# Optimization experiments

Hardware: AMD Instinct MI355X
Metric: run time of the kernel (lower is better)

## Reference

```python
import jax, jax.numpy as jnp
import numpy as np

B, S, H, NH = 2, 2048, 2048, 16
HD = H // NH  # 128
SCALE = HD ** -0.5


def rotate_half(x):
    x1, x2 = x[..., : x.shape[-1] // 2], x[..., x.shape[-1] // 2 :]
    return jnp.concatenate((-x2, x1), axis=-1)


def setup_inputs() -> dict:
    key = jax.random.key(0)
    ks = jax.random.split(key, 7)
    inv_freq = 1.0 / (10000.0 ** (np.arange(0, HD, 2, dtype=np.float32) / HD))
    t = np.arange(S, dtype=np.float32)
    freqs = np.outer(t, inv_freq)  # [S, HD/2]
    emb = np.concatenate([freqs, freqs], axis=-1)  # [S, HD]
    cos = jnp.asarray(np.cos(emb))[None, None]  # [1,1,S,HD]
    sin = jnp.asarray(np.sin(emb))[None, None]
    std = H ** -0.5
    return {
        "hidden_states": jax.random.normal(ks[0], (B, S, H), jnp.float32),
        "cos": cos,
        "sin": sin,
        "Wq": jax.random.normal(ks[1], (H, H), jnp.float32) * std,
        "Wk": jax.random.normal(ks[2], (H, H), jnp.float32) * std,
        "Wv": jax.random.normal(ks[3], (H, H), jnp.float32) * std,
        "Wo": jax.random.normal(ks[4], (H, H), jnp.float32) * std,
    }


def reference(hidden_states, cos, sin, Wq, Wk, Wv, Wo):
    b, s, _ = hidden_states.shape
    # projections (torch F.linear: x @ W.T), reshape to [b, nh, s, hd]
    def proj(W):
        y = jnp.einsum("bsh,oh->bso", hidden_states, W)
        return y.reshape(b, s, NH, HD).transpose(0, 2, 1, 3)

    q, k, v = proj(Wq), proj(Wk), proj(Wv)
    # rotary embedding
    q = q * cos + rotate_half(q) * sin
    k = k * cos + rotate_half(k) * sin
    # attention: scores [b, nh, s, s]
    scores = jnp.einsum("bhqd,bhkd->bhqk", q, k) * SCALE
    causal_mask = jnp.triu(jnp.full((s, s), -jnp.inf, dtype=scores.dtype), k=1)
    scores = scores + causal_mask
    attn = jax.nn.softmax(scores, axis=-1)
    out = jnp.einsum("bhqk,bhkd->bhqd", attn, v)
    out = out.transpose(0, 2, 1, 3).reshape(b, s, NH * HD)
    return jnp.einsum("bso,ho->bsh", out, Wo)
```

## Files before the change

### kernel.cpp

```cpp
#include <hip/hip_runtime.h>

typedef unsigned short u16;
typedef unsigned int   u32;
typedef __attribute__((ext_vector_type(8))) __bf16 bf16x8;
typedef __attribute__((ext_vector_type(8))) unsigned short u16x8;
typedef __attribute__((ext_vector_type(4))) float f32x4;

#define DEVINL static __device__ __forceinline__
#define MFMA16(a,b,c) __builtin_amdgcn_mfma_f32_16x16x32_bf16((a),(b),(c),0,0,0)

#define GLOAD16(g, l) __builtin_amdgcn_global_load_lds( \
    (const __attribute__((address_space(1))) void*)(g), \
    (__attribute__((address_space(3))) void*)(l), 16, 0, 0)

constexpr float ATT_SCALE = 0.08838834764831845f;

DEVINL u16 f2bf(float f) {
  union { float f; u32 u; } v; v.f = f;
  u32 r = v.u + 0x7fffu + ((v.u >> 16) & 1u);
  return (u16)(r >> 16);
}

struct CvtArgs {
  const float* src[5];
  u16*         dst[5];
  int          nblk[5];
};

__global__ __launch_bounds__(256) void cvt_bf16(CvtArgs a) {
  const int z = blockIdx.y;
  if (blockIdx.x >= a.nblk[z]) return;
  const size_t i = ((size_t)blockIdx.x * 256 + threadIdx.x) * 8;
  const float* s = a.src[z] + i;
  float4 x0 = *(const float4*)(s);
  float4 x1 = *(const float4*)(s + 4);
  u16x8 r;
  r[0]=f2bf(x0.x); r[1]=f2bf(x0.y); r[2]=f2bf(x0.z); r[3]=f2bf(x0.w);
  r[4]=f2bf(x1.x); r[5]=f2bf(x1.y); r[6]=f2bf(x1.z); r[7]=f2bf(x1.w);
  *(u16x8*)(a.dst[z] + i) = r;
}

#define SLOT_U16 24576
#define A_HALF_U16 8192
#define B_OFF_U16 16384
#define B_HALF_U16 4096

#define STAGE_AH(s, half, ktile) do {                                          \
    _Pragma("unroll")                                                          \
    for (int it_ = 0; it_ < 2; ++it_) {                                        \
      const u32 p_  = it_*512 + t;                                             \
      const u32 gl_ = p_ ^ ((p_ >> 3) & 7u);                                   \
      GLOAD16(A + (size_t)(bm*256 + (half)*128 + (gl_ >> 3))*2048              \
                 + (ktile)*64 + (gl_ & 7u)*8,                                  \
              &lds[(s)*SLOT_U16 + (half)*A_HALF_U16 + p_*8]);                  \
    } } while (0)

#define STAGE_BH(s, half, ktile) do {                                          \
    const u32 p_  = (u32)t;                                                    \
    const u32 gl_ = p_ ^ ((p_ >> 3) & 7u);                                     \
    GLOAD16(Wg + (size_t)(bnl*128 + (half)*64 + (gl_ >> 3))*2048               \
               + (ktile)*64 + (gl_ & 7u)*8,                                    \
            &lds[(s)*SLOT_U16 + B_OFF_U16 + (half)*B_HALF_U16 + p_*8]);        \
  } while (0)

#define LDA(s, mfg, ks) (*(const bf16x8*)&lds[(s)*SLOT_U16 + wm*A_HALF_U16 +   \
    ((((mfg)*16 + c)*64 + (ks)*32 + qq*8) ^ ((u32)(c & 7) << 3))])
#define LDB(s, nf, ks)  (*(const bf16x8*)&lds[(s)*SLOT_U16 + B_OFF_U16 +       \
    (nf)*B_HALF_U16 + (((wn*16 + c)*64 + (ks)*32 + qq*8) ^ ((u32)(c & 7) << 3))])

#define PHASE(s, mq, ks, LOADB, VMW, ...) do {                                 \
    if (LOADB) { bfr0 = LDB(s, 0, ks); bfr1 = LDB(s, 1, ks); }                 \
    bf16x8 a0_ = LDA(s, (mq)*4+0, ks);                                         \
    bf16x8 a1_ = LDA(s, (mq)*4+1, ks);                                         \
    bf16x8 a2_ = LDA(s, (mq)*4+2, ks);                                         \
    bf16x8 a3_ = LDA(s, (mq)*4+3, ks);                                         \
    __VA_ARGS__;                                                               \
    if (VMW) { asm volatile("s_waitcnt vmcnt(6)" ::: "memory"); }              \
    __builtin_amdgcn_s_barrier();                                              \
    asm volatile("s_waitcnt lgkmcnt(0)" ::: "memory");                         \
    __builtin_amdgcn_sched_barrier(0);                                         \
    __builtin_amdgcn_s_setprio(1);                                             \
    acc[(mq)*4+0][0] = MFMA16(a0_, bfr0, acc[(mq)*4+0][0]);                    \
    acc[(mq)*4+1][0] = MFMA16(a1_, bfr0, acc[(mq)*4+1][0]);                    \
    acc[(mq)*4+2][0] = MFMA16(a2_, bfr0, acc[(mq)*4+2][0]);                    \
    acc[(mq)*4+3][0] = MFMA16(a3_, bfr0, acc[(mq)*4+3][0]);                    \
    acc[(mq)*4+0][1] = MFMA16(a0_, bfr1, acc[(mq)*4+0][1]);                    \
    acc[(mq)*4+1][1] = MFMA16(a1_, bfr1, acc[(mq)*4+1][1]);                    \
    acc[(mq)*4+2][1] = MFMA16(a2_, bfr1, acc[(mq)*4+2][1]);                    \
    acc[(mq)*4+3][1] = MFMA16(a3_, bfr1, acc[(mq)*4+3][1]);                    \
    __builtin_amdgcn_s_setprio(0);                                             \
    __builtin_amdgcn_s_barrier();                                              \
  } while (0)

template<int FUSED>
__global__ __launch_bounds__(512, 1)
void gemm8(const u16* __restrict__ A, const u16* __restrict__ W0,
           const u16* __restrict__ W1, const u16* __restrict__ W2,
           u16* __restrict__ outq, u16* __restrict__ outk,
           u16* __restrict__ outv, float* __restrict__ outf,
           const float* __restrict__ cosp, const float* __restrict__ sinp)
{
  __shared__ __attribute__((aligned(16))) u16 lds[3*SLOT_U16];

  const int t = threadIdx.x;
  const int lane = t & 63, w = t >> 6;
  const int wm = w >> 2, wn = w & 3;
  const int c = lane & 15, qq = lane >> 4;
  const int bm = blockIdx.x, bn = blockIdx.y;
  const int z   = FUSED ? (bn >> 4) : 3;
  const int bnl = FUSED ? (bn & 15) : bn;
  const u16* Wg = FUSED ? (z == 0 ? W0 : (z == 1 ? W1 : W2)) : W0;

  f32x4 acc[8][2] = {};

  STAGE_AH(0, 0, 0); STAGE_AH(0, 1, 0); STAGE_BH(0, 0, 0); STAGE_BH(0, 1, 0);
  STAGE_AH(1, 0, 1); STAGE_AH(1, 1, 1); STAGE_BH(1, 0, 1); STAGE_BH(1, 1, 1);
  asm volatile("s_waitcnt vmcnt(6)" ::: "memory");
  __builtin_amdgcn_s_barrier();

  bf16x8 bfr0, bfr1;
  int slot = 0;
  #pragma unroll 1
  for (int i = 0; i < 32; ++i) {
    const int s2 = (slot >= 1) ? slot - 1 : 2;
    const int tn = (i < 30) ? i + 2 : 31;
    PHASE(slot, 0, 0, 1, 0, STAGE_AH(s2, 0, tn));
    PHASE(slot, 1, 0, 0, 0, STAGE_AH(s2, 1, tn));
    PHASE(slot, 0, 1, 1, 0, STAGE_BH(s2, 0, tn); STAGE_BH(s2, 1, tn));
    PHASE(slot, 1, 1, 0, 1, );
    slot = (slot == 2) ? 0 : slot + 1;
  }

  __syncthreads();

  if (!FUSED) {
    #pragma unroll
    for (int mfg = 0; mfg < 8; ++mfg)
      #pragma unroll
      for (int nf = 0; nf < 2; ++nf)
        #pragma unroll
        for (int r = 0; r < 4; ++r) {
          int row = bm*256 + wm*128 + mfg*16 + qq*4 + r;
          int col = bnl*128 + nf*64 + wn*16 + c;
          outf[(size_t)row*2048 + col] = acc[mfg][nf][r];
        }
    return;
  }

  if (z <= 1) {
    u16* qk = (z == 0) ? outq : outk;
    const int d1 = wn*16 + c, d2 = d1 + 64;
    #pragma unroll
    for (int mfg = 0; mfg < 8; ++mfg)
      #pragma unroll
      for (int r = 0; r < 4; ++r) {
        int m  = bm*256 + wm*128 + mfg*16 + qq*4 + r;
        int bb = m >> 11, s = m & 2047;
        const float* cs = cosp + s*128;
        const float* sn = sinp + s*128;
        u16* orow = qk + ((size_t)(bb*16 + bnl)*2048 + s)*128;
        float v1 = acc[mfg][0][r], v2 = acc[mfg][1][r];
        orow[d1] = f2bf(v1*cs[d1] - v2*sn[d1]);
        orow[d2] = f2bf(v2*cs[d2] + v1*sn[d2]);
      }
  } else {
    #pragma unroll
    for (int mfg = 0; mfg < 8; ++mfg)
      #pragma unroll
      for (int nf = 0; nf < 2; ++nf)
        #pragma unroll
        for (int r = 0; r < 4; ++r)
          lds[(nf*64 + wn*16 + c)*264 + wm*128 + mfg*16 + qq*4 + r] =
              f2bf(acc[mfg][nf][r]);
    __syncthreads();
    const int d = t >> 2, seg = t & 3;
    const int bb = bm >> 3, s0 = (bm & 7) * 256;
    u16* og = outv + ((size_t)(bb*16 + bnl)*128 + d)*2048 + s0 + seg*64;
    #pragma unroll
    for (int j = 0; j < 8; ++j)
      *(u16x8*)&og[j*8] = *(const u16x8*)&lds[d*264 + seg*64 + j*8];
  }
}

__global__ __launch_bounds__(256, 2)
void attn_fwd(const u16* __restrict__ qw, const u16* __restrict__ kw,
              const u16* __restrict__ vw, u16* __restrict__ ow)
{
  __shared__ __attribute__((aligned(16))) u16 Klds[2][64*128];
  __shared__ __attribute__((aligned(16))) u16 Vlds[2][128*64];
  __shared__ __attribute__((aligned(16))) u16 Plds[4][16*72];

  const int t = threadIdx.x, lane = t & 63, w = t >> 6;
  const int c = lane & 15, qq = lane >> 4;
  const int ip = blockIdx.x, h = blockIdx.y, b = blockIdx.z;
  const int qlo = ip, qhi = 31 - ip;

  const size_t bh = (size_t)b*16 + h;
  const u16* Qg = qw + bh*(2048*128);
  const u16* Kg = kw + bh*(2048*128);
  const u16* Vg = vw + bh*(128*2048);
  u16* pw = &Plds[w][0];

  bf16x8 qf_hi[4], qf_lo[4];
  {
    const u16* qh = Qg + (size_t)(qhi*64 + w*16 + c)*128;
    const u16* ql = Qg + (size_t)(qlo*64 + w*16 + c)*128;
    #pragma unroll
    for (int ds = 0; ds < 4; ++ds) {
      qf_hi[ds] = *(const bf16x8*)(qh + ds*32 + qq*8);
      qf_lo[ds] = *(const bf16x8*)(ql + ds*32 + qq*8);
    }
  }

  float m_hi[4] = {-1e30f,-1e30f,-1e30f,-1e30f};
  float l_hi[4] = {0.f,0.f,0.f,0.f};
  f32x4 o_hi[8] = {};
  float m_lo[4] = {-1e30f,-1e30f,-1e30f,-1e30f};
  float l_lo[4] = {0.f,0.f,0.f,0.f};
  f32x4 o_lo[8] = {};

#define ASTAGE(BUF, KT) do {                                                  \
    const u16* kbase = Kg + (size_t)(KT)*8192;                                \
    _Pragma("unroll")                                                         \
    for (int it = 0; it < 4; ++it) {                                          \
      const u32 p  = it*256 + t;                                              \
      const u32 gl = p ^ ((p >> 4) & 7u);                                     \
      GLOAD16(kbase + gl*8, &Klds[BUF][p*8]);                                 \
    }                                                                         \
    _Pragma("unroll")                                                         \
    for (int it = 0; it < 4; ++it) {                                          \
      const u32 p  = it*256 + t;                                              \
      const u32 gl = p ^ ((p >> 3) & 7u);                                     \
      GLOAD16(Vg + (size_t)(gl >> 3)*2048 + (KT)*64 + (gl & 7u)*8,            \
              &Vlds[BUF][p*8]);                                               \
    }                                                                         \
  } while (0)

#define APROCESS(QF, OACC, MR, LR, QBASE, DIAG, BUF) do {                     \
    f32x4 sc[4] = {};                                                         \
    __builtin_amdgcn_s_setprio(1);                                            \
    _Pragma("unroll")                                                         \
    for (int ds = 0; ds < 4; ++ds) {                                          \
      _Pragma("unroll")                                                       \
      for (int nj = 0; nj < 4; ++nj) {                                        \
        const u32 row = nj*16 + c;                                            \
        const u32 p = (row*128 + ds*32 + qq*8) ^ ((row & 7u) << 3);           \
        bf16x8 kb = *(const bf16x8*)&Klds[BUF][p];                            \
        sc[nj] = MFMA16(QF[ds], kb, sc[nj]);                                  \
      }                                                                       \
    }                                                                         \
    __builtin_amdgcn_s_setprio(0);                                            \
    const int qg0 = (QBASE) + w*16 + qq*4;                                    \
    float escale[4];                                                          \
    _Pragma("unroll")                                                         \
    for (int r = 0; r < 4; ++r) {                                             \
      float mx = -1e30f;                                                      \
      _Pragma("unroll")                                                       \
      for (int nj = 0; nj < 4; ++nj) {                                        \
        float s = sc[nj][r] * ATT_SCALE;                                      \
        if ((DIAG) && (kt*64 + nj*16 + c) > (qg0 + r)) s = -1e30f;            \
        sc[nj][r] = s;                                                        \
        mx = fmaxf(mx, s);                                                    \
      }                                                                       \
      mx = fmaxf(mx, __shfl_xor(mx, 1));                                      \
      mx = fmaxf(mx, __shfl_xor(mx, 2));                                      \
      mx = fmaxf(mx, __shfl_xor(mx, 4));                                      \
      mx = fmaxf(mx, __shfl_xor(mx, 8));                                      \
      float mnew = fmaxf(MR[r], mx);                                          \
      escale[r] = __expf(MR[r] - mnew);                                       \
      MR[r] = mnew;                                                           \
      float sum = 0.f;                                                        \
      _Pragma("unroll")                                                       \
      for (int nj = 0; nj < 4; ++nj) {                                        \
        float pv = __expf(sc[nj][r] - mnew);                                  \
        sum += pv;                                                            \
        pw[(qq*4 + r)*72 + nj*16 + c] = f2bf(pv);                             \
      }                                                                       \
      sum += __shfl_xor(sum, 1);                                              \
      sum += __shfl_xor(sum, 2);                                              \
      sum += __shfl_xor(sum, 4);                                              \
      sum += __shfl_xor(sum, 8);                                              \
      LR[r] = LR[r]*escale[r] + sum;                                          \
    }                                                                         \
    _Pragma("unroll")                                                         \
    for (int nj8 = 0; nj8 < 8; ++nj8)                                         \
      _Pragma("unroll")                                                       \
      for (int r = 0; r < 4; ++r)                                             \
        OACC[nj8][r] *= escale[r];                                            \
    __builtin_amdgcn_s_setprio(1);                                            \
    _Pragma("unroll")                                                         \
    for (int ks = 0; ks < 2; ++ks) {                                          \
      bf16x8 pa = *(const bf16x8*)&pw[c*72 + ks*32 + qq*8];                   \
      _Pragma("unroll")                                                       \
      for (int nj8 = 0; nj8 < 8; ++nj8) {                                     \
        const u32 row = nj8*16 + c;                                           \
        const u32 p = (row*64 + ks*32 + qq*8) ^ ((row & 7u) << 3);            \
        bf16x8 vb = *(const bf16x8*)&Vlds[BUF][p];                            \
        OACC[nj8] = MFMA16(pa, vb, OACC[nj8]);                                \
      }                                                                       \
    }                                                                         \
    __builtin_amdgcn_s_setprio(0);                                            \
  } while (0)

  ASTAGE(0, 0);
  for (int kt = 0; kt <= qhi; ++kt) {
    const int cur = kt & 1;
    __syncthreads();
    if (kt < qhi) ASTAGE(cur ^ 1, kt + 1);
    APROCESS(qf_hi, o_hi, m_hi, l_hi, qhi*64, (kt == qhi), cur);
    if (kt <= qlo)
      APROCESS(qf_lo, o_lo, m_lo, l_lo, qlo*64, (kt == qlo), cur);
  }

#undef ASTAGE
#undef APROCESS

  {
    float inv[4];
    #pragma unroll
    for (int r = 0; r < 4; ++r) inv[r] = 1.0f / l_hi[r];
    u16* og = ow + ((size_t)b*2048 + qhi*64 + w*16)*2048 + h*128;
    #pragma unroll
    for (int nj8 = 0; nj8 < 8; ++nj8)
      #pragma unroll
      for (int r = 0; r < 4; ++r)
        og[(size_t)(qq*4 + r)*2048 + nj8*16 + c] = f2bf(o_hi[nj8][r]*inv[r]);
  }
  {
    float inv[4];
    #pragma unroll
    for (int r = 0; r < 4; ++r) inv[r] = 1.0f / l_lo[r];
    u16* og = ow + ((size_t)b*2048 + qlo*64 + w*16)*2048 + h*128;
    #pragma unroll
    for (int nj8 = 0; nj8 < 8; ++nj8)
      #pragma unroll
      for (int r = 0; r < 4; ++r)
        og[(size_t)(qq*4 + r)*2048 + nj8*16 + c] = f2bf(o_lo[nj8][r]*inv[r]);
  }
}

extern "C" void kernel_launch(void* const* d_in, const int* in_sizes, int n_in,
                              void* d_out, int out_size, void* d_ws, size_t ws_size,
                              hipStream_t stream)
{
  const float* hs   = (const float*)d_in[0];
  const float* cosp = (const float*)d_in[1];
  const float* sinp = (const float*)d_in[2];
  const float* Wq   = (const float*)d_in[3];
  const float* Wk   = (const float*)d_in[4];
  const float* Wv   = (const float*)d_in[5];
  const float* Wo   = (const float*)d_in[6];

  u16* q_ws  = (u16*)d_ws;
  u16* k_ws  = q_ws  + 8388608;
  u16* vt_ws = k_ws  + 8388608;
  u16* ao_ws = vt_ws + 8388608;
  u16* hs_b  = ao_ws + 8388608;
  u16* wq_b  = hs_b  + 8388608;
  u16* wk_b  = wq_b  + 4194304;
  u16* wv_b  = wk_b  + 4194304;
  u16* wo_b  = wv_b  + 4194304;

  CvtArgs ca;
  ca.src[0]=hs; ca.src[1]=Wq; ca.src[2]=Wk; ca.src[3]=Wv; ca.src[4]=Wo;
  ca.dst[0]=hs_b; ca.dst[1]=wq_b; ca.dst[2]=wk_b; ca.dst[3]=wv_b; ca.dst[4]=wo_b;
  ca.nblk[0]=4096; ca.nblk[1]=2048; ca.nblk[2]=2048; ca.nblk[3]=2048; ca.nblk[4]=2048;

  cvt_bf16<<<dim3(4096, 5), dim3(256), 0, stream>>>(ca);

  gemm8<1><<<dim3(16, 48), dim3(512), 0, stream>>>(
      hs_b, wq_b, wk_b, wv_b, q_ws, k_ws, vt_ws, nullptr, cosp, sinp);

  attn_fwd<<<dim3(16, 16, 2), dim3(256), 0, stream>>>(q_ws, k_ws, vt_ws, ao_ws);

  gemm8<0><<<dim3(16, 16), dim3(512), 0, stream>>>(
      ao_ws, wo_b, nullptr, nullptr, nullptr, nullptr, nullptr,
      (float*)d_out, nullptr, nullptr);
}
```

Baseline: 399.0 us.

## Enlarge GEMM tiles to 256x256 with ten-slot LDS ring and XCD-aware block remap

The projection GEMMs move from a 256x128 tile to a 256x256 tile per workgroup, so each wave now holds 8x4 accumulator fragments. This raises arithmetic intensity and halves the number of blocks. Loads are staged as 128-row panels into a 10-slot LDS ring with a deeper prefetch distance and adjusted vmcnt waits. Blocks use a 1D grid remapped so that consecutive tiles land on the same XCD, which should improve L2 reuse. The risks are higher register pressure, since 128 accumulator floats per lane sit alongside an LDS footprint of about 160KB, and fewer blocks than CUs on the output projection (128 blocks).

Measured after the change: 434.7 us. 1.09x slower.

```diff
diff --git a/kernel.cpp b/kernel.cpp
--- a/kernel.cpp
+++ b/kernel.cpp
@@ -12,6 +12,8 @@
 #define GLOAD16(g, l) __builtin_amdgcn_global_load_lds( \
     (const __attribute__((address_space(1))) void*)(g), \
     (__attribute__((address_space(3))) void*)(l), 16, 0, 0)
+
+#define VMC(N) asm volatile("s_waitcnt vmcnt(" #N ")" ::: "memory")
 
 constexpr float ATT_SCALE = 0.08838834764831845f;
 
@@ -40,108 +42,117 @@
   *(u16x8*)(a.dst[z] + i) = r;
 }
 
-#define SLOT_U16 24576
-#define A_HALF_U16 8192
-#define B_OFF_U16 16384
-#define B_HALF_U16 4096
-
-#define STAGE_AH(s, half, ktile) do {                                          \
+
+#define STAGEU(SL, TI, PA) do {                                                \
     _Pragma("unroll")                                                          \
-    for (int it_ = 0; it_ < 2; ++it_) {                                        \
-      const u32 p_  = it_*512 + t;                                             \
+    for (int i_ = 0; i_ < 2; ++i_) {                                           \
+      const u32 p_  = i_*512 + t;                                              \
       const u32 gl_ = p_ ^ ((p_ >> 3) & 7u);                                   \
-      GLOAD16(A + (size_t)(bm*256 + (half)*128 + (gl_ >> 3))*2048              \
-                 + (ktile)*64 + (gl_ & 7u)*8,                                  \
-              &lds[(s)*SLOT_U16 + (half)*A_HALF_U16 + p_*8]);                  \
+      const u16* s_ = ((PA) < 2)                                               \
+        ? Ag + (size_t)(bm*256 + (PA)*128 + (gl_ >> 3))*2048                   \
+             + (TI)*64 + (gl_ & 7u)*8                                          \
+        : Wg + (size_t)(bnl*256 + ((PA)-2)*128 + (gl_ >> 3))*2048              \
+             + (TI)*64 + (gl_ & 7u)*8;                                         \
+      GLOAD16(s_, &lds[(SL)*8192 + p_*8]);                                     \
     } } while (0)
 
-#define STAGE_BH(s, half, ktile) do {                                          \
-    const u32 p_  = (u32)t;                                                    \
-    const u32 gl_ = p_ ^ ((p_ >> 3) & 7u);                                     \
-    GLOAD16(Wg + (size_t)(bnl*128 + (half)*64 + (gl_ >> 3))*2048               \
-               + (ktile)*64 + (gl_ & 7u)*8,                                    \
-            &lds[(s)*SLOT_U16 + B_OFF_U16 + (half)*B_HALF_U16 + p_*8]);        \
-  } while (0)
-
-#define LDA(s, mfg, ks) (*(const bf16x8*)&lds[(s)*SLOT_U16 + wm*A_HALF_U16 +   \
-    ((((mfg)*16 + c)*64 + (ks)*32 + qq*8) ^ ((u32)(c & 7) << 3))])
-#define LDB(s, nf, ks)  (*(const bf16x8*)&lds[(s)*SLOT_U16 + B_OFF_U16 +       \
-    (nf)*B_HALF_U16 + (((wn*16 + c)*64 + (ks)*32 + qq*8) ^ ((u32)(c & 7) << 3))])
-
-#define PHASE(s, mq, ks, LOADB, VMW, ...) do {                                 \
-    if (LOADB) { bfr0 = LDB(s, 0, ks); bfr1 = LDB(s, 1, ks); }                 \
-    bf16x8 a0_ = LDA(s, (mq)*4+0, ks);                                         \
-    bf16x8 a1_ = LDA(s, (mq)*4+1, ks);                                         \
-    bf16x8 a2_ = LDA(s, (mq)*4+2, ks);                                         \
-    bf16x8 a3_ = LDA(s, (mq)*4+3, ks);                                         \
-    __VA_ARGS__;                                                               \
-    if (VMW) { asm volatile("s_waitcnt vmcnt(6)" ::: "memory"); }              \
+#define LDAU(SL, MFG, KS) (*(const bf16x8*)&lds[((SL)*8192 +                   \
+    ((((MFG)*16 + c) << 6) + (KS)*32 + qq*8)) ^ ((u32)(c & 7) << 3)])
+#define LDBU(SL, NF, KS)  (*(const bf16x8*)&lds[((SL)*8192 +                   \
+    (((((NF)&1)*64 + wn*16 + c) << 6) + (KS)*32 + qq*8)) ^ ((u32)(c & 7) << 3)])
+
+DEVINL int subm10(int x) { return x >= 10 ? x - 10 : x; }
+
+#define GPHASE(P, Q, KS, LOADB) do {                                           \
+    const int sA_ = subm10(s_tile + wm);                                       \
+    bf16x8 a0_ = LDAU(sA_, (Q)*4+0, KS);                                       \
+    bf16x8 a1_ = LDAU(sA_, (Q)*4+1, KS);                                       \
+    bf16x8 a2_ = LDAU(sA_, (Q)*4+2, KS);                                       \
+    bf16x8 a3_ = LDAU(sA_, (Q)*4+3, KS);                                       \
+    if (LOADB) {                                                               \
+      const int sB0_ = subm10(s_tile + 2), sB1_ = subm10(s_tile + 3);          \
+      b0 = LDBU(sB0_, 0, KS); b1 = LDBU(sB0_, 1, KS);                          \
+      b2 = LDBU(sB1_, 2, KS); b3 = LDBU(sB1_, 3, KS);                          \
+    }                                                                          \
+    if (4*T + (P) <= 121)                                                      \
+      STAGEU(s_stage, T + 1 + (((P)+2)>>2), ((P)+2)&3);                        \
+    s_stage = (s_stage + 1 == 10) ? 0 : s_stage + 1;                           \
+    if ((P) == 3) { if (T < 30) VMC(4); else if (T == 30) VMC(0); }            \
     __builtin_amdgcn_s_barrier();                                              \
     asm volatile("s_waitcnt lgkmcnt(0)" ::: "memory");                         \
     __builtin_amdgcn_sched_barrier(0);                                         \
     __builtin_amdgcn_s_setprio(1);                                             \
-    acc[(mq)*4+0][0] = MFMA16(a0_, bfr0, acc[(mq)*4+0][0]);                    \
-    acc[(mq)*4+1][0] = MFMA16(a1_, bfr0, acc[(mq)*4+1][0]);                    \
-    acc[(mq)*4+2][0] = MFMA16(a2_, bfr0, acc[(mq)*4+2][0]);                    \
-    acc[(mq)*4+3][0] = MFMA16(a3_, bfr0, acc[(mq)*4+3][0]);                    \
-    acc[(mq)*4+0][1] = MFMA16(a0_, bfr1, acc[(mq)*4+0][1]);                    \
-    acc[(mq)*4+1][1] = MFMA16(a1_, bfr1, acc[(mq)*4+1][1]);                    \
-    acc[(mq)*4+2][1] = MFMA16(a2_, bfr1, acc[(mq)*4+2][1]);                    \
-    acc[(mq)*4+3][1] = MFMA16(a3_, bfr1, acc[(mq)*4+3][1]);                    \
+    acc[(Q)*4+0][0] = MFMA16(a0_, b0, acc[(Q)*4+0][0]);                        \
+    acc[(Q)*4+1][0] = MFMA16(a1_, b0, acc[(Q)*4+1][0]);                        \
+    acc[(Q)*4+2][0] = MFMA16(a2_, b0, acc[(Q)*4+2][0]);                        \
+    acc[(Q)*4+3][0] = MFMA16(a3_, b0, acc[(Q)*4+3][0]);                        \
+    acc[(Q)*4+0][1] = MFMA16(a0_, b1, acc[(Q)*4+0][1]);                        \
+    acc[(Q)*4+1][1] = MFMA16(a1_, b1, acc[(Q)*4+1][1]);                        \
+    acc[(Q)*4+2][1] = MFMA16(a2_, b1, acc[(Q)*4+2][1]);                        \
+    acc[(Q)*4+3][1] = MFMA16(a3_, b1, acc[(Q)*4+3][1]);                        \
+    acc[(Q)*4+0][2] = MFMA16(a0_, b2, acc[(Q)*4+0][2]);                        \
+    acc[(Q)*4+1][2] = MFMA16(a1_, b2, acc[(Q)*4+1][2]);                        \
+    acc[(Q)*4+2][2] = MFMA16(a2_, b2, acc[(Q)*4+2][2]);                        \
+    acc[(Q)*4+3][2] = MFMA16(a3_, b2, acc[(Q)*4+3][2]);                        \
+    acc[(Q)*4+0][3] = MFMA16(a0_, b3, acc[(Q)*4+0][3]);                        \
+    acc[(Q)*4+1][3] = MFMA16(a1_, b3, acc[(Q)*4+1][3]);                        \
+    acc[(Q)*4+2][3] = MFMA16(a2_, b3, acc[(Q)*4+2][3]);                        \
+    acc[(Q)*4+3][3] = MFMA16(a3_, b3, acc[(Q)*4+3][3]);                        \
     __builtin_amdgcn_s_setprio(0);                                             \
     __builtin_amdgcn_s_barrier();                                              \
   } while (0)
 
 template<int FUSED>
 __global__ __launch_bounds__(512, 1)
-void gemm8(const u16* __restrict__ A, const u16* __restrict__ W0,
+void gemm9(const u16* __restrict__ Ag, const u16* __restrict__ W0,
            const u16* __restrict__ W1, const u16* __restrict__ W2,
            u16* __restrict__ outq, u16* __restrict__ outk,
            u16* __restrict__ outv, float* __restrict__ outf,
            const float* __restrict__ cosp, const float* __restrict__ sinp)
 {
-  __shared__ __attribute__((aligned(16))) u16 lds[3*SLOT_U16];
+  __shared__ __attribute__((aligned(16))) u16 lds[10 * 8192];
 
   const int t = threadIdx.x;
   const int lane = t & 63, w = t >> 6;
   const int wm = w >> 2, wn = w & 3;
   const int c = lane & 15, qq = lane >> 4;
-  const int bm = blockIdx.x, bn = blockIdx.y;
-  const int z   = FUSED ? (bn >> 4) : 3;
-  const int bnl = FUSED ? (bn & 15) : bn;
+
+  const int cpx = gridDim.x >> 3;
+  const int bid = blockIdx.x;
+  const int wg  = (bid & 7) * cpx + (bid >> 3);
+  const int bm  = wg & 15;
+  const int bnf = wg >> 4;
+  const int z   = FUSED ? (bnf >> 3) : 3;
+  const int bnl = FUSED ? (bnf & 7) : bnf;
   const u16* Wg = FUSED ? (z == 0 ? W0 : (z == 1 ? W1 : W2)) : W0;
 
-  f32x4 acc[8][2] = {};
-
-  STAGE_AH(0, 0, 0); STAGE_AH(0, 1, 0); STAGE_BH(0, 0, 0); STAGE_BH(0, 1, 0);
-  STAGE_AH(1, 0, 1); STAGE_AH(1, 1, 1); STAGE_BH(1, 0, 1); STAGE_BH(1, 1, 1);
-  asm volatile("s_waitcnt vmcnt(6)" ::: "memory");
+  f32x4 acc[8][4] = {};
+  bf16x8 b0, b1, b2, b3;
+
+  STAGEU(0, 0, 0); STAGEU(1, 0, 1); STAGEU(2, 0, 2); STAGEU(3, 0, 3);
+  STAGEU(4, 1, 0); STAGEU(5, 1, 1);
+  VMC(4);
   __builtin_amdgcn_s_barrier();
 
-  bf16x8 bfr0, bfr1;
-  int slot = 0;
+  int s_tile = 0, s_stage = 6;
   #pragma unroll 1
-  for (int i = 0; i < 32; ++i) {
-    const int s2 = (slot >= 1) ? slot - 1 : 2;
-    const int tn = (i < 30) ? i + 2 : 31;
-    PHASE(slot, 0, 0, 1, 0, STAGE_AH(s2, 0, tn));
-    PHASE(slot, 1, 0, 0, 0, STAGE_AH(s2, 1, tn));
-    PHASE(slot, 0, 1, 1, 0, STAGE_BH(s2, 0, tn); STAGE_BH(s2, 1, tn));
-    PHASE(slot, 1, 1, 0, 1, );
-    slot = (slot == 2) ? 0 : slot + 1;
-  }
-
-  __syncthreads();
+  for (int T = 0; T < 32; ++T) {
+    GPHASE(0, 0, 0, 1);
+    GPHASE(1, 1, 0, 0);
+    GPHASE(2, 0, 1, 1);
+    GPHASE(3, 1, 1, 0);
+    s_tile = subm10(s_tile + 4);
+  }
 
   if (!FUSED) {
     #pragma unroll
     for (int mfg = 0; mfg < 8; ++mfg)
       #pragma unroll
-      for (int nf = 0; nf < 2; ++nf)
+      for (int nf = 0; nf < 4; ++nf)
         #pragma unroll
         for (int r = 0; r < 4; ++r) {
           int row = bm*256 + wm*128 + mfg*16 + qq*4 + r;
-          int col = bnl*128 + nf*64 + wn*16 + c;
+          int col = bnl*256 + nf*64 + wn*16 + c;
           outf[(size_t)row*2048 + col] = acc[mfg][nf][r];
         }
     return;
@@ -158,27 +169,34 @@
         int bb = m >> 11, s = m & 2047;
         const float* cs = cosp + s*128;
         const float* sn = sinp + s*128;
-        u16* orow = qk + ((size_t)(bb*16 + bnl)*2048 + s)*128;
-        float v1 = acc[mfg][0][r], v2 = acc[mfg][1][r];
-        orow[d1] = f2bf(v1*cs[d1] - v2*sn[d1]);
-        orow[d2] = f2bf(v2*cs[d2] + v1*sn[d2]);
+        #pragma unroll
+        for (int h = 0; h < 2; ++h) {
+          u16* orow = qk + ((size_t)(bb*16 + bnl*2 + h)*2048 + s)*128;
+          float v1 = acc[mfg][2*h][r], v2 = acc[mfg][2*h+1][r];
+          orow[d1] = f2bf(v1*cs[d1] - v2*sn[d1]);
+          orow[d2] = f2bf(v2*cs[d2] + v1*sn[d2]);
+        }
       }
   } else {
+    __syncthreads();
     #pragma unroll
     for (int mfg = 0; mfg < 8; ++mfg)
       #pragma unroll
-      for (int nf = 0; nf < 2; ++nf)
+      for (int nf = 0; nf < 4; ++nf)
         #pragma unroll
-        for (int r = 0; r < 4; ++r)
-          lds[(nf*64 + wn*16 + c)*264 + wm*128 + mfg*16 + qq*4 + r] =
-              f2bf(acc[mfg][nf][r]);
+        for (int r = 0; r < 4; ++r) {
+          int cl = nf*64 + wn*16 + c;
+          int rl = wm*128 + mfg*16 + qq*4 + r;
+          lds[cl*264 + rl] = f2bf(acc[mfg][nf][r]);
+        }
     __syncthreads();
-    const int d = t >> 2, seg = t & 3;
+    const int cl = t >> 1, half = (t & 1) * 128;
     const int bb = bm >> 3, s0 = (bm & 7) * 256;
-    u16* og = outv + ((size_t)(bb*16 + bnl)*128 + d)*2048 + s0 + seg*64;
-    #pragma unroll
-    for (int j = 0; j < 8; ++j)
-      *(u16x8*)&og[j*8] = *(const u16x8*)&lds[d*264 + seg*64 + j*8];
+    const int head = bnl*2 + (cl >> 7), d = cl & 127;
+    u16* og = outv + ((size_t)(bb*16 + head)*128 + d)*2048 + s0 + half;
+    #pragma unroll
+    for (int j = 0; j < 16; ++j)
+      *(u16x8*)&og[j*8] = *(const u16x8*)&lds[cl*264 + half + j*8];
   }
 }
 
@@ -368,12 +386,12 @@
 
   cvt_bf16<<<dim3(4096, 5), dim3(256), 0, stream>>>(ca);
 
-  gemm8<1><<<dim3(16, 48), dim3(512), 0, stream>>>(
+  gemm9<1><<<dim3(384), dim3(512), 0, stream>>>(
       hs_b, wq_b, wk_b, wv_b, q_ws, k_ws, vt_ws, nullptr, cosp, sinp);
 
   attn_fwd<<<dim3(16, 16, 2), dim3(256), 0, stream>>>(q_ws, k_ws, vt_ws, ao_ws);
 
-  gemm8<0><<<dim3(16, 16), dim3(512), 0, stream>>>(
+  gemm9<0><<<dim3(128), dim3(512), 0, stream>>>(
       ao_ws, wo_b, nullptr, nullptr, nullptr, nullptr, nullptr,
       (float*)d_out, nullptr, nullptr);
 }
```
